# Performance work log

Measured on AMD Instinct MI355X. Metric: run time of the kernel, lower is better.

## Reference

```python
import jax, jax.numpy as jnp
import numpy as np

B, T, D, H = 4096, 200, 128, 16
NEG = -4294967295.0  # -2**32 + 1, as in the TF source


def setup_inputs() -> dict:
    key = jax.random.key(0)
    k1, k2, k3, k4, k5 = jax.random.split(key, 5)
    query = jax.random.normal(k1, (B, D), dtype=jnp.float32)
    facts = jax.random.normal(k2, (B, T, D), dtype=jnp.float32)
    mask = jax.random.randint(k3, (B, T), 0, 2).astype(bool)
    mask = mask.at[:, 0].set(True)  # ensure at least one valid position per row
    W1 = jax.random.normal(k4, (4 * D, H), dtype=jnp.float32) * (1.0 / np.sqrt(4 * D))
    b1 = jnp.zeros((H,), dtype=jnp.float32)
    W2 = jax.random.normal(k5, (H, 1), dtype=jnp.float32) * (1.0 / np.sqrt(H))
    b2 = jnp.zeros((1,), dtype=jnp.float32)
    return {"query": query, "facts": facts, "mask": mask,
            "W1": W1, "b1": b1, "W2": W2, "b2": b2}


def reference(query, facts, mask, W1, b1, W2, b2):
    # query: [B, D], facts: [B, T, D], mask: [B, T] bool
    q = jnp.broadcast_to(query[:, None, :], facts.shape)          # [B, T, D]
    din_all = jnp.concatenate([q, facts, q - facts, q * facts], axis=-1)  # [B, T, 4D]
    h = jax.nn.sigmoid(jnp.einsum('btf,fh->bth', din_all, W1) + b1)       # [B, T, H]
    scores = (jnp.einsum('bth,ho->bto', h, W2) + b2)[..., 0]              # [B, T]
    scores = jnp.where(mask, scores, NEG)
    attn = jax.nn.softmax(scores, axis=-1)                                 # [B, T]
    out = jnp.einsum('bt,btd->bd', attn, facts)                            # [B, D]
    return out
```

## Files before the change

kernel.cpp:

```cpp
#include <hip/hip_runtime.h>

#define B_DIM 4096
#define T_DIM 200
#define D_DIM 128
#define H_DIM 16
#define NCH   13

typedef _Float16 h2 __attribute__((ext_vector_type(2)));
typedef _Float16 h8 __attribute__((ext_vector_type(8)));
typedef __fp16   g2 __attribute__((ext_vector_type(2)));
typedef float    f4 __attribute__((ext_vector_type(4)));
union F8 { h8 v; h2 p[4]; unsigned int u[4]; };
union HU { unsigned int u; h2 h; };

__device__ __forceinline__ h2 pkh(float a, float b) {
    g2 t = __builtin_amdgcn_cvt_pkrtz(a, b);
    return __builtin_bit_cast(h2, t);
}
template<int CTRL>
__device__ __forceinline__ float dppmov(float x) {
    return __builtin_bit_cast(float,
        __builtin_amdgcn_update_dpp(0, __builtin_bit_cast(int, x), CTRL, 0xF, 0xF, true));
}
__device__ __forceinline__ float rorsum16(float x) {
    x += dppmov<0x121>(x);
    x += dppmov<0x122>(x);
    x += dppmov<0x124>(x);
    x += dppmov<0x128>(x);
    return x;
}

extern "C" __global__ __launch_bounds__(512)
void din_fused(const float* __restrict__ query,
               const float* __restrict__ facts,
               const int* __restrict__ mask,
               const float* __restrict__ W1,
               const float* __restrict__ b1,
               const float* __restrict__ W2,
               float* __restrict__ out)
{
    const int tid  = threadIdx.x;
    const int wid  = tid >> 6;
    const int lane = tid & 63;
    const int rl   = lane & 15;
    const int g    = lane >> 4;
    const int b    = blockIdx.x * 8 + wid;

    __shared__ float W1bc[H_DIM * D_DIM];
    __shared__ float W1dd[H_DIM * D_DIM];
    __shared__ float W1ac[H_DIM * D_DIM];
    __shared__ unsigned int wef[8][H_DIM * 64];
    __shared__ float qwl[8][H_DIM];
    __shared__ float wxch[8][16];

    const float* fb = facts + (size_t)b * (T_DIM * D_DIM);
    const int*   mb = mask  + (size_t)b * T_DIM;
    const float* qb = query + (size_t)b * D_DIM;

    float4 F[8];
    auto loadF = [&](int c) {
        int r = 16 * c + rl; if (r > T_DIM - 1) r = T_DIM - 1;
        const float* p = fb + r * D_DIM + 8 * g;
        #pragma unroll
        for (int s = 0; s < 4; ++s) {
            F[2*s]     = *(const float4*)(p + 32 * s);
            F[2*s + 1] = *(const float4*)(p + 32 * s + 4);
        }
    };
    loadF(0);

    unsigned long long bal0, bal1, bal2, bal3;
    {
        int m0 = mb[lane];
        int m1 = mb[64 + lane];
        int m2 = mb[128 + lane];
        int m3 = (lane < 8) ? mb[192 + lane] : 0;
        bal0 = __ballot(m0 != 0);
        bal1 = __ballot(m1 != 0);
        bal2 = __ballot(m2 != 0);
        bal3 = __ballot(m3 != 0);
    }

    #pragma unroll
    for (int i = 0; i < 4; ++i) {
        int idx = tid * 4 + i;
        int h = idx >> 7, d = idx & 127;
        W1bc[idx] = W1[(128 + d) * H_DIM + h] - W1[(256 + d) * H_DIM + h];
        W1dd[idx] = W1[(384 + d) * H_DIM + h];
        W1ac[idx] = W1[d * H_DIM + h] + W1[(256 + d) * H_DIM + h];
    }
    __syncthreads();

    {
        int h = lane & 15, dg = lane >> 4;
        float p = 0.f;
        #pragma unroll
        for (int k = 0; k < 8; ++k) {
            float4 a4 = *(const float4*)&W1ac[h * D_DIM + dg * 32 + 4 * k];
            float4 q4 = *(const float4*)(qb + dg * 32 + 4 * k);
            p += a4.x * q4.x + a4.y * q4.y + a4.z * q4.z + a4.w * q4.w;
        }
        p += __shfl_xor(p, 16);
        p += __shfl_xor(p, 32);
        if (lane < 16) qwl[wid][h] = p + b1[h];
    }
    #pragma unroll
    for (int pass = 0; pass < 2; ++pass) {
        int h  = 8 * pass + (lane >> 3);
        int p0 = (lane & 7) * 8;
        unsigned int pk[8];
        #pragma unroll
        for (int u = 0; u < 8; ++u) {
            int d0 = 2 * (p0 + u);
            float a0 = W1bc[h * D_DIM + d0]     + qb[d0]     * W1dd[h * D_DIM + d0];
            float a1 = W1bc[h * D_DIM + d0 + 1] + qb[d0 + 1] * W1dd[h * D_DIM + d0 + 1];
            HU t; t.h = pkh(a0, a1); pk[u] = t.u;
        }
        *(uint4*)&wef[wid][h * 64 + p0]     = make_uint4(pk[0], pk[1], pk[2], pk[3]);
        *(uint4*)&wef[wid][h * 64 + p0 + 4] = make_uint4(pk[4], pk[5], pk[6], pk[7]);
    }
    asm volatile("s_waitcnt lgkmcnt(0)" ::: "memory");

    F8 fB[4];
    #pragma unroll
    for (int s = 0; s < 4; ++s) {
        uint4 t = *(const uint4*)&wef[wid][rl * 64 + 16 * s + 4 * g];
        fB[s].u[0] = t.x; fB[s].u[1] = t.y; fB[s].u[2] = t.z; fB[s].u[3] = t.w;
    }
    const float qv  = qwl[wid][rl];
    const float w2v = W2[rl];

    float a32[32];
    #pragma unroll
    for (int i = 0; i < 32; ++i) a32[i] = 0.f;
    float lw = 0.f;

    #pragma unroll 1
    for (int c = 0; c < NCH; ++c) {
        F8 fa[4];
        #pragma unroll
        for (int s = 0; s < 4; ++s) {
            fa[s].p[0] = pkh(F[2*s].x,     F[2*s].y);
            fa[s].p[1] = pkh(F[2*s].z,     F[2*s].w);
            fa[s].p[2] = pkh(F[2*s + 1].x, F[2*s + 1].y);
            fa[s].p[3] = pkh(F[2*s + 1].z, F[2*s + 1].w);
        }
        if (c + 1 < NCH) loadF(c + 1);

        f4 D = {0.f, 0.f, 0.f, 0.f};
        D = __builtin_amdgcn_mfma_f32_16x16x32_f16(fa[0].v, fB[0].v, D, 0, 0, 0);
        D = __builtin_amdgcn_mfma_f32_16x16x32_f16(fa[1].v, fB[1].v, D, 0, 0, 0);
        D = __builtin_amdgcn_mfma_f32_16x16x32_f16(fa[2].v, fB[2].v, D, 0, 0, 0);
        D = __builtin_amdgcn_mfma_f32_16x16x32_f16(fa[3].v, fB[3].v, D, 0, 0, 0);

        int r0 = 16 * c;
        unsigned long long wrd = r0 < 64 ? bal0 : r0 < 128 ? bal1 : r0 < 192 ? bal2 : bal3;
        unsigned long long sw  = wrd >> ((r0 & 63) + 4 * g);

        float wj[4];
        #pragma unroll
        for (int j = 0; j < 4; ++j) {
            float sc = w2v / (1.f + __expf(-(qv + D[j])));
            sc = rorsum16(sc);
            wj[j] = ((sw >> j) & 1) ? __expf(sc) : 0.f;
        }
        lw += wj[0] + wj[1] + wj[2] + wj[3];

        if (rl == 0)
            *(float4*)&wxch[wid][4 * g] = make_float4(wj[0], wj[1], wj[2], wj[3]);
        asm volatile("s_waitcnt lgkmcnt(0)" ::: "memory");
        float wv = wxch[wid][rl];

        #pragma unroll
        for (int s = 0; s < 4; ++s)
            #pragma unroll
            for (int e = 0; e < 4; ++e) {
                a32[8*s + 2*e]     += wv * (float)fa[s].p[e].x;
                a32[8*s + 2*e + 1] += wv * (float)fa[s].p[e].y;
            }
    }

    float l = lw;
    l += __shfl_xor(l, 16);
    l += __shfl_xor(l, 32);
    float inv = 1.f / l;
    #pragma unroll
    for (int i = 0; i < 32; ++i) a32[i] = rorsum16(a32[i]);
    if (rl == 0) {
        float* ob = out + (size_t)b * D_DIM + 8 * g;
        #pragma unroll
        for (int s = 0; s < 4; ++s) {
            *(float4*)(ob + 32 * s) =
                make_float4(a32[8*s]*inv, a32[8*s+1]*inv, a32[8*s+2]*inv, a32[8*s+3]*inv);
            *(float4*)(ob + 32 * s + 4) =
                make_float4(a32[8*s+4]*inv, a32[8*s+5]*inv, a32[8*s+6]*inv, a32[8*s+7]*inv);
        }
    }
}

extern "C" void kernel_launch(void* const* d_in, const int* in_sizes, int n_in,
                              void* d_out, int out_size, void* d_ws, size_t ws_size,
                              hipStream_t stream) {
    const float* query = (const float*)d_in[0];
    const float* facts = (const float*)d_in[1];
    const int*   mask  = (const int*)d_in[2];
    const float* W1    = (const float*)d_in[3];
    const float* b1    = (const float*)d_in[4];
    const float* W2    = (const float*)d_in[5];
    float* out = (float*)d_out;
    (void)in_sizes; (void)n_in; (void)out_size; (void)d_ws; (void)ws_size;

    din_fused<<<dim3(B_DIM / 8), dim3(512), 0, stream>>>(
        query, facts, mask, W1, b1, W2, out);
}
```

Baseline: 93.45 us.

## Deepen facts prefetch to 1.5 chunks with rotating half-buffers, keep B operand in LDS

The facts prefetch is split into half-chunk buffers rotated across three register sets, so loads run about one and a half chunks ahead instead of one. The loop is manually unrolled by three to keep the buffer rotation static. The fixed MFMA B-operand fragments now stay in LDS in a lane-linear layout and are reloaded each chunk, which frees registers for the extra prefetch buffers. In exchange it adds LDS reads per chunk and more code size.

```diff
diff --git a/kernel.cpp b/kernel.cpp
--- a/kernel.cpp
+++ b/kernel.cpp
@@ -12,6 +12,7 @@
 typedef float    f4 __attribute__((ext_vector_type(4)));
 union F8 { h8 v; h2 p[4]; unsigned int u[4]; };
 union HU { unsigned int u; h2 h; };
+union U4F8 { uint4 q; h8 v; };
 
 __device__ __forceinline__ h2 pkh(float a, float b) {
     g2 t = __builtin_amdgcn_cvt_pkrtz(a, b);
@@ -49,7 +50,7 @@
     __shared__ float W1bc[H_DIM * D_DIM];
     __shared__ float W1dd[H_DIM * D_DIM];
     __shared__ float W1ac[H_DIM * D_DIM];
-    __shared__ unsigned int wef[8][H_DIM * 64];
+    __shared__ unsigned int pool[8][1024];
     __shared__ float qwl[8][H_DIM];
     __shared__ float wxch[8][16];
 
@@ -57,17 +58,17 @@
     const int*   mb = mask  + (size_t)b * T_DIM;
     const float* qb = query + (size_t)b * D_DIM;
 
-    float4 F[8];
-    auto loadF = [&](int c) {
+    float4 H0[4], H1[4], H2[4];
+    auto loadH = [&](int m, float4 (&H)[4]) {
+        int c = m >> 1, sp = (m & 1) * 2;
         int r = 16 * c + rl; if (r > T_DIM - 1) r = T_DIM - 1;
-        const float* p = fb + r * D_DIM + 8 * g;
-        #pragma unroll
-        for (int s = 0; s < 4; ++s) {
-            F[2*s]     = *(const float4*)(p + 32 * s);
-            F[2*s + 1] = *(const float4*)(p + 32 * s + 4);
-        }
+        const float* p = fb + r * D_DIM + 8 * g + 32 * sp;
+        H[0] = *(const float4*)(p);
+        H[1] = *(const float4*)(p + 4);
+        H[2] = *(const float4*)(p + 32);
+        H[3] = *(const float4*)(p + 36);
     };
-    loadF(0);
+    loadH(0, H0); loadH(1, H1); loadH(2, H2);
 
     unsigned long long bal0, bal1, bal2, bal3;
     {
@@ -116,17 +117,23 @@
             float a1 = W1bc[h * D_DIM + d0 + 1] + qb[d0 + 1] * W1dd[h * D_DIM + d0 + 1];
             HU t; t.h = pkh(a0, a1); pk[u] = t.u;
         }
-        *(uint4*)&wef[wid][h * 64 + p0]     = make_uint4(pk[0], pk[1], pk[2], pk[3]);
-        *(uint4*)&wef[wid][h * 64 + p0 + 4] = make_uint4(pk[4], pk[5], pk[6], pk[7]);
+        *(uint4*)&pool[wid][h * 64 + p0]     = make_uint4(pk[0], pk[1], pk[2], pk[3]);
+        *(uint4*)&pool[wid][h * 64 + p0 + 4] = make_uint4(pk[4], pk[5], pk[6], pk[7]);
     }
     asm volatile("s_waitcnt lgkmcnt(0)" ::: "memory");
 
-    F8 fB[4];
-    #pragma unroll
-    for (int s = 0; s < 4; ++s) {
-        uint4 t = *(const uint4*)&wef[wid][rl * 64 + 16 * s + 4 * g];
-        fB[s].u[0] = t.x; fB[s].u[1] = t.y; fB[s].u[2] = t.z; fB[s].u[3] = t.w;
-    }
+    {
+        uint4 fBq[4];
+        #pragma unroll
+        for (int s = 0; s < 4; ++s)
+            fBq[s] = *(const uint4*)&pool[wid][rl * 64 + 16 * s + 4 * g];
+        asm volatile("s_waitcnt lgkmcnt(0)" ::: "memory");
+        #pragma unroll
+        for (int s = 0; s < 4; ++s)
+            *(uint4*)&pool[wid][s * 256 + lane * 4] = fBq[s];
+        asm volatile("s_waitcnt lgkmcnt(0)" ::: "memory");
+    }
+
     const float qv  = qwl[wid][rl];
     const float w2v = W2[rl];
 
@@ -135,23 +142,25 @@
     for (int i = 0; i < 32; ++i) a32[i] = 0.f;
     float lw = 0.f;
 
-    #pragma unroll 1
-    for (int c = 0; c < NCH; ++c) {
+    auto doChunk = [&](int c, float4 (&B0)[4], float4 (&B1)[4]) {
         F8 fa[4];
+        fa[0].p[0] = pkh(B0[0].x, B0[0].y); fa[0].p[1] = pkh(B0[0].z, B0[0].w);
+        fa[0].p[2] = pkh(B0[1].x, B0[1].y); fa[0].p[3] = pkh(B0[1].z, B0[1].w);
+        fa[1].p[0] = pkh(B0[2].x, B0[2].y); fa[1].p[1] = pkh(B0[2].z, B0[2].w);
+        fa[1].p[2] = pkh(B0[3].x, B0[3].y); fa[1].p[3] = pkh(B0[3].z, B0[3].w);
+        if (2 * c + 3 < 2 * NCH) loadH(2 * c + 3, B0);
+        fa[2].p[0] = pkh(B1[0].x, B1[0].y); fa[2].p[1] = pkh(B1[0].z, B1[0].w);
+        fa[2].p[2] = pkh(B1[1].x, B1[1].y); fa[2].p[3] = pkh(B1[1].z, B1[1].w);
+        fa[3].p[0] = pkh(B1[2].x, B1[2].y); fa[3].p[1] = pkh(B1[2].z, B1[2].w);
+        fa[3].p[2] = pkh(B1[3].x, B1[3].y); fa[3].p[3] = pkh(B1[3].z, B1[3].w);
+        if (2 * c + 4 < 2 * NCH) loadH(2 * c + 4, B1);
+
+        f4 D = {0.f, 0.f, 0.f, 0.f};
         #pragma unroll
         for (int s = 0; s < 4; ++s) {
-            fa[s].p[0] = pkh(F[2*s].x,     F[2*s].y);
-            fa[s].p[1] = pkh(F[2*s].z,     F[2*s].w);
-            fa[s].p[2] = pkh(F[2*s + 1].x, F[2*s + 1].y);
-            fa[s].p[3] = pkh(F[2*s + 1].z, F[2*s + 1].w);
-        }
-        if (c + 1 < NCH) loadF(c + 1);
-
-        f4 D = {0.f, 0.f, 0.f, 0.f};
-        D = __builtin_amdgcn_mfma_f32_16x16x32_f16(fa[0].v, fB[0].v, D, 0, 0, 0);
-        D = __builtin_amdgcn_mfma_f32_16x16x32_f16(fa[1].v, fB[1].v, D, 0, 0, 0);
-        D = __builtin_amdgcn_mfma_f32_16x16x32_f16(fa[2].v, fB[2].v, D, 0, 0, 0);
-        D = __builtin_amdgcn_mfma_f32_16x16x32_f16(fa[3].v, fB[3].v, D, 0, 0, 0);
+            U4F8 w; w.q = *(const uint4*)&pool[wid][s * 256 + lane * 4];
+            D = __builtin_amdgcn_mfma_f32_16x16x32_f16(fa[s].v, w.v, D, 0, 0, 0);
+        }
 
         int r0 = 16 * c;
         unsigned long long wrd = r0 < 64 ? bal0 : r0 < 128 ? bal1 : r0 < 192 ? bal2 : bal3;
@@ -178,7 +187,15 @@
                 a32[8*s + 2*e]     += wv * (float)fa[s].p[e].x;
                 a32[8*s + 2*e + 1] += wv * (float)fa[s].p[e].y;
             }
-    }
+    };
+
+    #pragma unroll 1
+    for (int cc = 0; cc + 2 < NCH; cc += 3) {
+        doChunk(cc,     H0, H1);
+        doChunk(cc + 1, H2, H0);
+        doChunk(cc + 2, H1, H2);
+    }
+    doChunk(12, H0, H1);
 
     float l = lw;
     l += __shfl_xor(l, 16);
```

Result: slower. 282.3 us (+202.1%).
